# Kernel tuning notes

Hardware: AMD Instinct MI355X
Metric: run time of the kernel (lower is better)

Reference implementation:

```python
import jax, jax.numpy as jnp
import numpy as np

D_MODEL = 1024
H = 16
D_K = D_MODEL // H
D_FF = 4096
EPS = 1e-6
NEG = -1e9


def layernorm(x, alpha, bias):
    # custom LN: unbiased std (ddof=1), scalar alpha/bias, divide by (std+eps)
    mean = jnp.mean(x, axis=-1, keepdims=True)
    n = x.shape[-1]
    var = jnp.sum((x - mean) ** 2, axis=-1, keepdims=True) / (n - 1)
    std = jnp.sqrt(var)
    return alpha * (x - mean) / (std + EPS) + bias


def setup_inputs() -> dict:
    key = jax.random.key(0)
    ks = jax.random.split(key, 16)
    B, S = 2, 2048
    s = 1.0 / np.sqrt(D_MODEL)
    inp = {
        "x": jax.random.normal(ks[0], (B, S, D_MODEL), jnp.float32),
        "src_mask": jnp.ones((B, 1, S), jnp.int32),
        "wq": jax.random.normal(ks[1], (D_MODEL, D_MODEL), jnp.float32) * s,
        "bq": jnp.zeros((D_MODEL,), jnp.float32),
        "wk": jax.random.normal(ks[2], (D_MODEL, D_MODEL), jnp.float32) * s,
        "bk": jnp.zeros((D_MODEL,), jnp.float32),
        "wv": jax.random.normal(ks[3], (D_MODEL, D_MODEL), jnp.float32) * s,
        "bv": jnp.zeros((D_MODEL,), jnp.float32),
        "wo": jax.random.normal(ks[4], (D_MODEL, D_MODEL), jnp.float32) * s,
        "bo": jnp.zeros((D_MODEL,), jnp.float32),
        "w1": jax.random.normal(ks[5], (D_MODEL, D_FF), jnp.float32) * s,
        "b1": jnp.zeros((D_FF,), jnp.float32),
        "w2": jax.random.normal(ks[6], (D_FF, D_MODEL), jnp.float32) * (1.0 / np.sqrt(D_FF)),
        "b2": jnp.zeros((D_MODEL,), jnp.float32),
        "ln1_a": jnp.ones((1,), jnp.float32),
        "ln1_b": jnp.zeros((1,), jnp.float32),
        "ln2_a": jnp.ones((1,), jnp.float32),
        "ln2_b": jnp.zeros((1,), jnp.float32),
    }
    return inp


def reference(x, src_mask, wq, bq, wk, bk, wv, bv, wo, bo,
              w1, b1, w2, b2, ln1_a, ln1_b, ln2_a, ln2_b):
    B, S, _ = x.shape
    # --- residual 1: pre-norm self attention ---
    xn = layernorm(x, ln1_a, ln1_b)
    q = (xn @ wq + bq).reshape(B, S, H, D_K)
    k = (xn @ wk + bk).reshape(B, S, H, D_K)
    v = (xn @ wv + bv).reshape(B, S, H, D_K)
    # scores [B, H, S, S]
    scores = jnp.einsum("bqhd,bkhd->bhqk", q, k) / jnp.sqrt(jnp.float32(D_K))
    m = src_mask[:, None, :, :]  # [B,1,1,S]
    scores = jnp.where(m == 0, NEG, scores)
    attn = jax.nn.softmax(scores, axis=-1)
    ctx = jnp.einsum("bhqk,bkhd->bqhd", attn, v).reshape(B, S, D_MODEL)
    attn_out = ctx @ wo + bo
    x = x + attn_out
    # --- residual 2: pre-norm FFN ---
    xn = layernorm(x, ln2_a, ln2_b)
    ff = jax.nn.relu(xn @ w1 + b1) @ w2 + b2
    return x + ff
```

## Files before the change

kernel.cpp:

```cpp
#include <hip/hip_runtime.h>
#include <hip/hip_bf16.h>

typedef __attribute__((ext_vector_type(8))) short short8;
typedef __attribute__((ext_vector_type(4))) float f32x4;
typedef __attribute__((ext_vector_type(4))) unsigned int u32x4;
using u16 = unsigned short;
typedef unsigned int u32;

__device__ __forceinline__ u16 f2bf(float f) {
    u32 u = __builtin_bit_cast(u32, f);
    u32 r = u + 0x7FFFu + ((u >> 16) & 1u);
    return (u16)(r >> 16);
}

__device__ __forceinline__ float exp2fast(float x) {
    return __builtin_amdgcn_exp2f(x);
}

__device__ __forceinline__ u32 cvtpk(float lo, float hi) {
    u32 r;
    asm("v_cvt_pk_bf16_f32 %0, %1, %2" : "=v"(r) : "v"(lo), "v"(hi));
    return r;
}

__device__ __forceinline__ void async_load16(const void* g, void* l) {
    __builtin_amdgcn_global_load_lds(
        (const __attribute__((address_space(1))) void*)g,
        (__attribute__((address_space(3))) void*)l, 16, 0, 0);
}

__device__ __forceinline__ void wg_barrier() {
    asm volatile("" ::: "memory");
    __builtin_amdgcn_s_barrier();
    asm volatile("" ::: "memory");
}

__global__ __launch_bounds__(256) void convt_kernel(const float* __restrict__ w,
                                                    u16* __restrict__ wt, int K, int N) {
    __shared__ float tile[32][33];
    int bn = blockIdx.x * 32, bk = blockIdx.y * 32;
    int tx = threadIdx.x & 31, ty = threadIdx.x >> 5;
#pragma unroll
    for (int i = 0; i < 4; i++)
        tile[ty + i * 8][tx] = w[(size_t)(bk + ty + i * 8) * N + bn + tx];
    __syncthreads();
#pragma unroll
    for (int i = 0; i < 4; i++)
        wt[(size_t)(bn + ty + i * 8) * K + bk + tx] = f2bf(tile[tx][ty + i * 8]);
}

__global__ __launch_bounds__(256) void convt4_kernel(const float* __restrict__ wa,
                                                     const float* __restrict__ wb,
                                                     const float* __restrict__ wc,
                                                     const float* __restrict__ wd,
                                                     u16* __restrict__ da,
                                                     u16* __restrict__ db,
                                                     u16* __restrict__ dc,
                                                     u16* __restrict__ dd) {
    __shared__ float tile[32][33];
    int z = blockIdx.z;
    const float* w = (z == 0) ? wa : (z == 1) ? wb : (z == 2) ? wc : wd;
    u16* wt = (z == 0) ? da : (z == 1) ? db : (z == 2) ? dc : dd;
    int bn = blockIdx.x * 32, bk = blockIdx.y * 32;
    int tx = threadIdx.x & 31, ty = threadIdx.x >> 5;
#pragma unroll
    for (int i = 0; i < 4; i++)
        tile[ty + i * 8][tx] = w[(size_t)(bk + ty + i * 8) * 1024 + bn + tx];
    __syncthreads();
#pragma unroll
    for (int i = 0; i < 4; i++)
        wt[(size_t)(bn + ty + i * 8) * 1024 + bk + tx] = f2bf(tile[tx][ty + i * 8]);
}

__global__ __launch_bounds__(256) void vtrans_kernel(const u16* __restrict__ qkv,
                                                     u16* __restrict__ vT) {
    __shared__ u16 tile[32][33];
    int bs = blockIdx.x * 32;
    int bc = blockIdx.y * 32;
    int b  = blockIdx.z;
    int tx = threadIdx.x & 31, ty = threadIdx.x >> 5;
#pragma unroll
    for (int i = 0; i < 4; i++)
        tile[ty + i * 8][tx] = qkv[(size_t)(b * 2048 + bs + ty + i * 8) * 3072 + 2048 + bc + tx];
    __syncthreads();
#pragma unroll
    for (int i = 0; i < 4; i++)
        vT[(size_t)(b * 1024 + bc + ty + i * 8) * 2048 + bs + tx] = tile[tx][ty + i * 8];
}

__global__ __launch_bounds__(256) void ln_kernel(const float* __restrict__ x,
                                                 const float* __restrict__ ga,
                                                 const float* __restrict__ gb,
                                                 u16* __restrict__ out) {
    int row = blockIdx.x;
    const float4* xr = (const float4*)(x + (size_t)row * 1024);
    float4 v = xr[threadIdx.x];
    float s  = v.x + v.y + v.z + v.w;
    float s2 = v.x * v.x + v.y * v.y + v.z * v.z + v.w * v.w;
#pragma unroll
    for (int off = 32; off; off >>= 1) {
        s  += __shfl_down(s, off);
        s2 += __shfl_down(s2, off);
    }
    __shared__ float rs[4], rs2[4];
    int wid = threadIdx.x >> 6, lane = threadIdx.x & 63;
    if (lane == 0) { rs[wid] = s; rs2[wid] = s2; }
    __syncthreads();
    float S  = rs[0] + rs[1] + rs[2] + rs[3];
    float S2 = rs2[0] + rs2[1] + rs2[2] + rs2[3];
    float mean = S * (1.0f / 1024.0f);
    float var  = fmaxf((S2 - 1024.0f * mean * mean) * (1.0f / 1023.0f), 0.0f);
    float scale = ga[0] / (sqrtf(var) + 1e-6f);
    float shift = gb[0] - mean * scale;
    u16 h0 = f2bf(v.x * scale + shift);
    u16 h1 = f2bf(v.y * scale + shift);
    u16 h2 = f2bf(v.z * scale + shift);
    u16 h3 = f2bf(v.w * scale + shift);
    uint2 pv;
    pv.x = (u32)h0 | ((u32)h1 << 16);
    pv.y = (u32)h2 | ((u32)h3 << 16);
    *(uint2*)(out + (size_t)row * 1024 + threadIdx.x * 4) = pv;
}

__global__ __launch_bounds__(256) void bias3_kernel(const float* __restrict__ a,
                                                    const float* __restrict__ b,
                                                    const float* __restrict__ c,
                                                    float* __restrict__ d) {
    int i = blockIdx.x * 256 + threadIdx.x;
    float v = (i < 1024) ? a[i] : ((i < 2048) ? b[i - 1024] : c[i - 2048]);
    d[i] = v;
}

__global__ __launch_bounds__(256) void addbias_kernel(float* __restrict__ dst,
                                                      const float* __restrict__ p,
                                                      const float* __restrict__ bias,
                                                      const float* __restrict__ resid) {
    int i4 = blockIdx.x * 256 + threadIdx.x;
    float4 d  = ((const float4*)dst)[i4];
    float4 pp = ((const float4*)p)[i4];
    float4 rr = ((const float4*)resid)[i4];
    float4 bb = *(const float4*)(bias + ((i4 * 4) & 1023));
    d.x += pp.x + bb.x + rr.x;
    d.y += pp.y + bb.y + rr.y;
    d.z += pp.z + bb.z + rr.z;
    d.w += pp.w + bb.w + rr.w;
    ((float4*)dst)[i4] = d;
}

__global__ __launch_bounds__(256) void addbias2_ln_kernel(float* __restrict__ dst,
                                                          const float* __restrict__ p0,
                                                          const float* __restrict__ p1,
                                                          const float* __restrict__ bias,
                                                          const float* __restrict__ resid,
                                                          const float* __restrict__ ga,
                                                          const float* __restrict__ gb,
                                                          u16* __restrict__ xn) {
    int row = blockIdx.x;
    int i4 = row * 256 + threadIdx.x;
    float4 d  = ((const float4*)dst)[i4];
    float4 pa = ((const float4*)p0)[i4];
    float4 pb = ((const float4*)p1)[i4];
    float4 rr = ((const float4*)resid)[i4];
    float4 bb = *(const float4*)(bias + threadIdx.x * 4);
    d.x += pa.x + pb.x + bb.x + rr.x;
    d.y += pa.y + pb.y + bb.y + rr.y;
    d.z += pa.z + pb.z + bb.z + rr.z;
    d.w += pa.w + pb.w + bb.w + rr.w;
    ((float4*)dst)[i4] = d;

    float s  = d.x + d.y + d.z + d.w;
    float s2 = d.x * d.x + d.y * d.y + d.z * d.z + d.w * d.w;
#pragma unroll
    for (int off = 32; off; off >>= 1) {
        s  += __shfl_down(s, off);
        s2 += __shfl_down(s2, off);
    }
    __shared__ float rs[4], rs2[4];
    int wid = threadIdx.x >> 6, lane = threadIdx.x & 63;
    if (lane == 0) { rs[wid] = s; rs2[wid] = s2; }
    __syncthreads();
    float S  = rs[0] + rs[1] + rs[2] + rs[3];
    float S2 = rs2[0] + rs2[1] + rs2[2] + rs2[3];
    float mean = S * (1.0f / 1024.0f);
    float var  = fmaxf((S2 - 1024.0f * mean * mean) * (1.0f / 1023.0f), 0.0f);
    float scale = ga[0] / (sqrtf(var) + 1e-6f);
    float shift = gb[0] - mean * scale;
    uint2 pv;
    pv.x = (u32)f2bf(d.x * scale + shift) | ((u32)f2bf(d.y * scale + shift) << 16);
    pv.y = (u32)f2bf(d.z * scale + shift) | ((u32)f2bf(d.w * scale + shift) << 16);
    *(uint2*)(xn + (size_t)row * 1024 + threadIdx.x * 4) = pv;
}

template <int RELU>
__global__ __launch_bounds__(512) void gemm256_bt(const u16* __restrict__ A,
                                                  const u16* __restrict__ Bt,
                                                  const float* __restrict__ bias,
                                                  u16* __restrict__ C,
                                                  int M, int N, int K, int tilesN) {
    __shared__ u16 lds[2][2][16384];
    const int tid = threadIdx.x;
    const int lane = tid & 63, wid = tid >> 6;
    const int l15 = lane & 15, l4 = lane >> 4;
    const int wm = wid >> 2, wn = wid & 3;

    int nwg = gridDim.x;
    int bid = blockIdx.x;
    int swz = (bid & 7) * (nwg >> 3) + (bid >> 3);
    int ty = swz / tilesN, tx = swz % tilesN;

    const u16* Ag = A + (size_t)(ty * 256) * K;
    const u16* Bg = Bt + (size_t)(tx * 256) * K;

    auto stage_half = [&](int slot, int ab, int half, const u16* G, int k0) {
#pragma unroll
        for (int j = 0; j < 2; j++) {
            int off16 = half * 1024 + j * 512 + tid;
            int r = off16 >> 3;
            int gs = (off16 & 7) ^ (r & 7);
            const u16* src = G + (size_t)r * K + k0 + gs * 8;
            u16* dst = &lds[slot][ab][(size_t)(half * 1024 + j * 512 + (wid << 6)) * 8];
            async_load16(src, dst);
        }
    };

    f32x4 acc[8][4] = {};
    const int nT = K >> 6;

    stage_half(0, 0, 0, Ag, 0);
    stage_half(0, 0, 1, Ag, 0);
    stage_half(0, 1, 0, Bg, 0);
    stage_half(0, 1, 1, Bg, 0);
    __builtin_amdgcn_sched_barrier(0);

    for (int t = 0; t < nT; ++t) {
        const int cs = t & 1, ns = cs ^ 1;
        const int k1 = (t + 1) << 6;
        const bool pf = (t + 1 < nT);
#pragma unroll
        for (int ph = 0; ph < 4; ++ph) {
            if (ph == 0 && pf) { stage_half(ns, 0, 0, Ag, k1); stage_half(ns, 0, 1, Ag, k1); }
            if (ph == 1 && pf) { stage_half(ns, 1, 0, Bg, k1); stage_half(ns, 1, 1, Bg, k1); }
            __builtin_amdgcn_sched_barrier(0);
            if (ph == 0) {
                if (pf) asm volatile("s_waitcnt vmcnt(4)" ::: "memory");
                else    asm volatile("s_waitcnt vmcnt(0)" ::: "memory");
            }
            wg_barrier();

            const int rh = ph >> 1, ch = ph & 1;
            const u16* la = &lds[cs][0][0];
            const u16* lb = &lds[cs][1][0];
            short8 af[4][2], bf[2][2];
#pragma unroll
            for (int m2 = 0; m2 < 4; m2++) {
                int ra = wm * 128 + rh * 64 + m2 * 16 + l15;
#pragma unroll
                for (int ks = 0; ks < 2; ks++) {
                    int sl = (l4 + ks * 4) ^ (ra & 7);
                    af[m2][ks] = *(const short8*)&la[ra * 64 + sl * 8];
                }
            }
#pragma unroll
            for (int n2 = 0; n2 < 2; n2++) {
                int rb = wn * 64 + ch * 32 + n2 * 16 + l15;
#pragma unroll
                for (int ks = 0; ks < 2; ks++) {
                    int sl = (l4 + ks * 4) ^ (rb & 7);
                    bf[n2][ks] = *(const short8*)&lb[rb * 64 + sl * 8];
                }
            }
            __builtin_amdgcn_s_setprio(1);
#pragma unroll
            for (int m2 = 0; m2 < 4; m2++)
#pragma unroll
                for (int n2 = 0; n2 < 2; n2++)
#pragma unroll
                    for (int ks = 0; ks < 2; ks++)
                        acc[rh * 4 + m2][ch * 2 + n2] = __builtin_amdgcn_mfma_f32_16x16x32_bf16(
                            af[m2][ks], bf[n2][ks], acc[rh * 4 + m2][ch * 2 + n2], 0, 0, 0);
            __builtin_amdgcn_s_setprio(0);
            wg_barrier();
        }
    }

#pragma unroll
    for (int mi = 0; mi < 8; mi++) {
        int row0 = ty * 256 + wm * 128 + (mi >> 2) * 64 + (mi & 3) * 16 + l4 * 4;
#pragma unroll
        for (int ni = 0; ni < 4; ni++) {
            int col = tx * 256 + wn * 64 + (ni >> 1) * 32 + (ni & 1) * 16 + l15;
            float bc = bias[col];
#pragma unroll
            for (int jj = 0; jj < 4; jj++) {
                float v = acc[mi][ni][jj] + bc;
                if (RELU) v = fmaxf(v, 0.0f);
                C[(size_t)(row0 + jj) * N + col] = f2bf(v);
            }
        }
    }
}

template <int MODE, int RELU, int RESID>
__global__ __launch_bounds__(256) void gemm_bt(const u16* __restrict__ A,
                                               const u16* __restrict__ Bt,
                                               const float* __restrict__ bias,
                                               void* __restrict__ C0,
                                               void* __restrict__ C1,
                                               void* __restrict__ Cp1,
                                               const float* __restrict__ resid,
                                               int M, int N, int K, int kLen) {
    __shared__ u16 As[8192];
    __shared__ u16 Bs[8192];
    int tid = threadIdx.x, lane = tid & 63, wid = tid >> 6;
    int l15 = lane & 15, l4 = lane >> 4;
    int rowA0 = blockIdx.x * 128;
    int rowB0 = blockIdx.y * 128;
    int kOff = blockIdx.z * kLen;
    int len = K - kOff; if (len > kLen) len = kLen;
    void* Cout = (blockIdx.z == gridDim.z - 1) ? C1 : (blockIdx.z == 0 ? C0 : Cp1);
    int waveM = wid >> 1, waveN = wid & 1;

    int fl = tid * 8;
    int r0 = fl >> 5, c0 = fl & 31;
    const u16* gA0 = A + (size_t)(rowA0 + r0) * K + c0 + kOff;
    const u16* gA1 = A + (size_t)(rowA0 + 64 + r0) * K + c0 + kOff;
    const u16* gB0 = Bt + (size_t)(rowB0 + r0) * K + c0 + kOff;
    const u16* gB1 = Bt + (size_t)(rowB0 + 64 + r0) * K + c0 + kOff;

    f32x4 acc[4][4] = {};
    const int nIter = len >> 5;

    async_load16(gA0, As + wid * 512);
    async_load16(gA1, As + 2048 + wid * 512);
    async_load16(gB0, Bs + wid * 512);
    async_load16(gB1, Bs + 2048 + wid * 512);

    int cur = 0, kb = 32;
    for (int it = 0; it < nIter; ++it) {
        asm volatile("s_waitcnt vmcnt(0)" ::: "memory");
        __builtin_amdgcn_s_barrier();
        if (it + 1 < nIter) {
            u16* a = As + (cur ^ 1) * 4096;
            u16* bb = Bs + (cur ^ 1) * 4096;
            async_load16(gA0 + kb, a + wid * 512);
            async_load16(gA1 + kb, a + 2048 + wid * 512);
            async_load16(gB0 + kb, bb + wid * 512);
            async_load16(gB1 + kb, bb + 2048 + wid * 512);
        }
        __builtin_amdgcn_sched_barrier(0);

        const u16* a = As + cur * 4096;
        const u16* bb = Bs + cur * 4096;
        short8 af[4], bf[4];
#pragma unroll
        for (int m = 0; m < 4; m++)
            af[m] = *(const short8*)&a[(waveM * 64 + m * 16 + l15) * 32 + l4 * 8];
#pragma unroll
        for (int n = 0; n < 4; n++)
            bf[n] = *(const short8*)&bb[(waveN * 64 + n * 16 + l15) * 32 + l4 * 8];
#pragma unroll
        for (int m = 0; m < 4; m++)
#pragma unroll
            for (int n = 0; n < 4; n++)
                acc[m][n] = __builtin_amdgcn_mfma_f32_16x16x32_bf16(af[m], bf[n], acc[m][n], 0, 0, 0);

        __builtin_amdgcn_s_barrier();
        cur ^= 1;
        kb += 32;
    }

#pragma unroll
    for (int m = 0; m < 4; m++) {
        int row = rowA0 + waveM * 64 + m * 16 + l4 * 4;
#pragma unroll
        for (int n = 0; n < 4; n++) {
            int col = rowB0 + waveN * 64 + n * 16 + l15;
            float bc = (MODE == 2) ? 0.0f : bias[col];
#pragma unroll
            for (int j = 0; j < 4; j++) {
                float v = acc[m][n][j] + bc;
                if (RELU) v = fmaxf(v, 0.0f);
                if (RESID) v += resid[(size_t)(row + j) * N + col];
                if (MODE == 1)
                    ((u16*)Cout)[(size_t)(row + j) * N + col] = f2bf(v);
                else
                    ((float*)Cout)[(size_t)(row + j) * N + col] = v;
            }
        }
    }
}

__global__ __launch_bounds__(512) void attn_kernel(const u16* __restrict__ qkv,
                                                   const u16* __restrict__ vT,
                                                   const int* __restrict__ mask,
                                                   u16* __restrict__ ctx) {
    const int S = 2048;
    const float C = 0.180336880f;
    int qt = blockIdx.x;
    int bh = blockIdx.y;
    int b = bh >> 4, h = bh & 15;
    int tid = threadIdx.x;
    int wid = tid >> 6, lane = tid & 63;
    int l15 = lane & 15, l4 = lane >> 4;
    int g = wid >> 2, qw = wid & 3;

    __shared__ u16 Ks[2][64][72];
    __shared__ u16 Vs[2][64][72];
    __shared__ u32 PT[8][16][38];
    __shared__ float mbuf[2][4][16], lbuf[2][4][16];
    __shared__ int mflag;

    if (tid == 0) mflag = 1;
    __syncthreads();
    {
        const int* mrow = mask + b * S;
        int ok = 1;
#pragma unroll
        for (int i = 0; i < 4; i++) ok &= (mrow[tid * 4 + i] != 0);
        if (!ok) mflag = 0;
    }

    int qrow0 = qt * 64 + qw * 16;
    const u16* qb = qkv + (size_t)(b * S + qrow0) * 3072 + h * 64;
    short8 qf0 = *(const short8*)(qb + (size_t)l15 * 3072 + l4 * 8);
    short8 qf1 = *(const short8*)(qb + (size_t)l15 * 3072 + 32 + l4 * 8);

    f32x4 o[4] = {};
    float m_i = -1e30f, lp = 0.0f;
    __syncthreads();
    const int allones = mflag;
    const int* mrow = mask + b * S;

    int tl = tid & 255;
    int srow = tl >> 3, c8 = (tl & 7) * 8;
    const int kt0 = g * 16;
    short8 kreg[2], vreg[2];
#pragma unroll
    for (int p = 0; p < 2; p++) {
        int r = p * 32 + srow;
        kreg[p] = *(const short8*)(qkv + (size_t)(b * S + kt0 * 64 + r) * 3072 + 1024 + h * 64 + c8);
        vreg[p] = *(const short8*)(vT + (size_t)(bh * 64 + r) * 2048 + kt0 * 64 + c8);
    }

    for (int it = 0; it < 16; ++it) {
        const int kt = kt0 + it;
        wg_barrier();
#pragma unroll
        for (int p = 0; p < 2; p++) {
            int r = p * 32 + srow;
            *(short8*)&Ks[g][r][c8] = kreg[p];
            *(short8*)&Vs[g][r][c8] = vreg[p];
        }
        if (it + 1 < 16) {
#pragma unroll
            for (int p = 0; p < 2; p++) {
                int r = p * 32 + srow;
                kreg[p] = *(const short8*)(qkv + (size_t)(b * S + (kt + 1) * 64 + r) * 3072 + 1024 + h * 64 + c8);
                vreg[p] = *(const short8*)(vT + (size_t)(bh * 64 + r) * 2048 + (kt + 1) * 64 + c8);
            }
        }
        asm volatile("s_waitcnt lgkmcnt(0)" ::: "memory");
        wg_barrier();

        float sc[4][4];
#pragma unroll
        for (int kc = 0; kc < 4; kc++) {
            short8 kf0 = *(const short8*)&Ks[g][kc * 16 + l15][l4 * 8];
            short8 kf1 = *(const short8*)&Ks[g][kc * 16 + l15][32 + l4 * 8];
            f32x4 a = {};
            a = __builtin_amdgcn_mfma_f32_16x16x32_bf16(kf0, qf0, a, 0, 0, 0);
            a = __builtin_amdgcn_mfma_f32_16x16x32_bf16(kf1, qf1, a, 0, 0, 0);
            if (allones) {
#pragma unroll
                for (int j = 0; j < 4; j++) sc[kc][j] = a[j];
            } else {
#pragma unroll
                for (int j = 0; j < 4; j++) {
                    int mk = mrow[kt * 64 + kc * 16 + l4 * 4 + j];
                    sc[kc][j] = mk ? a[j] : -1e9f;
                }
            }
        }

        float lm = sc[0][0];
#pragma unroll
        for (int kc = 0; kc < 4; kc++)
#pragma unroll
            for (int j = 0; j < 4; j++) lm = fmaxf(lm, sc[kc][j]);
        if (!__all(lm <= m_i + 64.0f)) {
            float t = lm;
            t = fmaxf(t, __shfl_xor(t, 16));
            t = fmaxf(t, __shfl_xor(t, 32));
            float newm = fmaxf(m_i, t);
            float r = exp2fast((m_i - newm) * C);
            lp *= r;
            float rr0 = __shfl(r, l4 * 4 + 0);
            float rr1 = __shfl(r, l4 * 4 + 1);
            float rr2 = __shfl(r, l4 * 4 + 2);
            float rr3 = __shfl(r, l4 * 4 + 3);
#pragma unroll
            for (int dc = 0; dc < 4; dc++) {
                o[dc][0] *= rr0; o[dc][1] *= rr1; o[dc][2] *= rr2; o[dc][3] *= rr3;
            }
            m_i = newm;
        }

        float nb = -m_i * C;
#pragma unroll
        for (int kc = 0; kc < 4; kc++) {
            float p0 = exp2fast(fmaf(sc[kc][0], C, nb));
            float p1 = exp2fast(fmaf(sc[kc][1], C, nb));
            float p2 = exp2fast(fmaf(sc[kc][2], C, nb));
            float p3 = exp2fast(fmaf(sc[kc][3], C, nb));
            lp += (p0 + p1) + (p2 + p3);
            uint2 w;
            w.x = cvtpk(p0, p1);
            w.y = cvtpk(p2, p3);
            *(uint2*)&PT[wid][l15][kc * 8 + l4 * 2] = w;
        }

        uint2 r01 = *(const uint2*)&PT[wid][l15][l4 * 4];
        uint2 r23 = *(const uint2*)&PT[wid][l15][l4 * 4 + 2];
        uint2 r45 = *(const uint2*)&PT[wid][l15][16 + l4 * 4];
        uint2 r67 = *(const uint2*)&PT[wid][l15][16 + l4 * 4 + 2];
        u32x4 w0 = {r01.x, r01.y, r23.x, r23.y};
        u32x4 w1 = {r45.x, r45.y, r67.x, r67.y};
        short8 pa0 = __builtin_bit_cast(short8, w0);
        short8 pa1 = __builtin_bit_cast(short8, w1);

#pragma unroll
        for (int dc = 0; dc < 4; dc++) {
            short8 vf0 = *(const short8*)&Vs[g][dc * 16 + l15][l4 * 8];
            short8 vf1 = *(const short8*)&Vs[g][dc * 16 + l15][32 + l4 * 8];
            o[dc] = __builtin_amdgcn_mfma_f32_16x16x32_bf16(pa0, vf0, o[dc], 0, 0, 0);
            o[dc] = __builtin_amdgcn_mfma_f32_16x16x32_bf16(pa1, vf1, o[dc], 0, 0, 0);
        }
    }

    float lt = lp;
    lt += __shfl_xor(lt, 16);
    lt += __shfl_xor(lt, 32);
    if (l4 == 0) { mbuf[g][qw][l15] = m_i; lbuf[g][qw][l15] = lt; }
    __syncthreads();
    float mo = mbuf[g ^ 1][qw][l15], lo = lbuf[g ^ 1][qw][l15];
    float M  = fmaxf(m_i, mo);
    float rs = exp2fast((m_i - M) * C);
    float ro = exp2fast((mo - M) * C);
    float inv = 1.0f / (rs * lt + ro * lo);
    float rs_j[4], iv_j[4];
#pragma unroll
    for (int j = 0; j < 4; j++) {
        rs_j[j] = __shfl(rs,  l4 * 4 + j);
        iv_j[j] = __shfl(inv, l4 * 4 + j);
    }

    float* obuf = (float*)&Ks[0][0][0];
#pragma unroll
    for (int c = 0; c < 2; c++) {
        int dce = (g ^ 1) * 2 + c;
#pragma unroll
        for (int j = 0; j < 4; j++)
            obuf[(((g * 4 + qw) * 16) + l4 * 4 + j) * 32 + c * 16 + l15] = o[dce][j] * rs_j[j];
    }
    __syncthreads();
#pragma unroll
    for (int c = 0; c < 2; c++) {
        int dco = g * 2 + c;
#pragma unroll
        for (int j = 0; j < 4; j++) {
            float peer = obuf[((((g ^ 1) * 4 + qw) * 16) + l4 * 4 + j) * 32 + c * 16 + l15];
            float val = (o[dco][j] * rs_j[j] + peer) * iv_j[j];
            int row = qrow0 + l4 * 4 + j;
            ctx[(size_t)(b * S + row) * 1024 + h * 64 + dco * 16 + l15] = f2bf(val);
        }
    }
}

extern "C" void kernel_launch(void* const* d_in, const int* in_sizes, int n_in,
                              void* d_out, int out_size, void* d_ws, size_t ws_size,
                              hipStream_t stream) {
    const float* x    = (const float*)d_in[0];
    const int*   mask = (const int*)d_in[1];
    const float* wq   = (const float*)d_in[2];
    const float* bq   = (const float*)d_in[3];
    const float* wk   = (const float*)d_in[4];
    const float* bk   = (const float*)d_in[5];
    const float* wv   = (const float*)d_in[6];
    const float* bv   = (const float*)d_in[7];
    const float* wo   = (const float*)d_in[8];
    const float* bo   = (const float*)d_in[9];
    const float* w1   = (const float*)d_in[10];
    const float* b1   = (const float*)d_in[11];
    const float* w2   = (const float*)d_in[12];
    const float* b2   = (const float*)d_in[13];
    const float* ln1a = (const float*)d_in[14];
    const float* ln1b = (const float*)d_in[15];
    const float* ln2a = (const float*)d_in[16];
    const float* ln2b = (const float*)d_in[17];
    float* out = (float*)d_out;

    char* ws = (char*)d_ws;
    u16*   wqkvt = (u16*)(ws + 0);
    u16*   wot   = (u16*)(ws + 6291456);
    u16*   w1t   = (u16*)(ws + 8388608);
    u16*   w2t   = (u16*)(ws + 16777216);
    float* bqkv  = (float*)(ws + 25165824);
    char*  regA  = ws + 26214400;
    u16*   xn1   = (u16*)(regA + 0);
    u16*   vT    = (u16*)(regA + 0);
    u16*   qkv   = (u16*)(regA + 8388608);
    u16*   ctx   = (u16*)(regA + 33554432);
    float* p0wo  = (float*)(regA + 0);
    float* p1wo  = (float*)(regA + 16777216);
    float* x1    = (float*)(ws + 68157440);
    u16*   xn2   = (u16*)(regA + 0);
    u16*   ff1   = (u16*)(regA + 8388608);
    float* p0f2  = (float*)(ws + 0);

    dim3 blk(256);

    convt4_kernel<<<dim3(32, 32, 4), blk, 0, stream>>>(
        wq, wk, wv, wo, wqkvt, wqkvt + 1024 * 1024, wqkvt + 2048 * 1024, wot);
    convt_kernel<<<dim3(128, 32), blk, 0, stream>>>(w1, w1t, 1024, 4096);
    convt_kernel<<<dim3(32, 128), blk, 0, stream>>>(w2, w2t, 4096, 1024);
    bias3_kernel<<<dim3(12), blk, 0, stream>>>(bq, bk, bv, bqkv);

    ln_kernel<<<dim3(4096), blk, 0, stream>>>(x, ln1a, ln1b, xn1);
    gemm256_bt<0><<<dim3(192), dim3(512), 0, stream>>>(xn1, wqkvt, bqkv, qkv, 4096, 3072, 1024, 12);
    vtrans_kernel<<<dim3(64, 32, 2), blk, 0, stream>>>(qkv, vT);
    attn_kernel<<<dim3(32, 32), dim3(512), 0, stream>>>(qkv, vT, mask, ctx);
    gemm_bt<2, 0, 0><<<dim3(32, 8, 3), blk, 0, stream>>>(ctx, wot, nullptr, p0wo, x1, p1wo,
                                                         nullptr, 4096, 1024, 1024, 352);
    addbias2_ln_kernel<<<dim3(4096), blk, 0, stream>>>(x1, p0wo, p1wo, bo, x, ln2a, ln2b, xn2);

    gemm256_bt<1><<<dim3(256), dim3(512), 0, stream>>>(xn2, w1t, b1, ff1, 4096, 4096, 1024, 16);
    gemm_bt<2, 0, 0><<<dim3(32, 8, 2), blk, 0, stream>>>(ff1, w2t, nullptr, p0f2, out, nullptr,
                                                         nullptr, 4096, 1024, 4096, 2048);
    addbias_kernel<<<dim3(4096), blk, 0, stream>>>(out, p0f2, b2, x1);
}
```

Before: 271.3 us.

## Run FFN down-projection on 256x256 split-K GEMM with bf16 partials

The FFN second GEMM (K=4096) now runs on the larger 256x256 tile kernel, with split-K across 4 slices instead of the 128-tile kernel with 2-way split. Three slices write bf16 partial sums and the last writes fp32 into the output. A reduction kernel sums the bf16 partials with bias and residual. The aim is more reuse per tile and less partial-sum traffic. The bf16 partials lose some precision.

```diff
diff --git a/kernel.cpp b/kernel.cpp
--- a/kernel.cpp
+++ b/kernel.cpp
@@ -11,6 +11,13 @@
     u32 u = __builtin_bit_cast(u32, f);
     u32 r = u + 0x7FFFu + ((u >> 16) & 1u);
     return (u16)(r >> 16);
+}
+
+__device__ __forceinline__ float bf2f(u32 w) {
+    return __builtin_bit_cast(float, w << 16);
+}
+__device__ __forceinline__ float bf2f_hi(u32 w) {
+    return __builtin_bit_cast(float, w & 0xFFFF0000u);
 }
 
 __device__ __forceinline__ float exp2fast(float x) {
@@ -131,19 +138,23 @@
     d[i] = v;
 }
 
-__global__ __launch_bounds__(256) void addbias_kernel(float* __restrict__ dst,
-                                                      const float* __restrict__ p,
-                                                      const float* __restrict__ bias,
-                                                      const float* __restrict__ resid) {
+__global__ __launch_bounds__(256) void addbias3b_kernel(float* __restrict__ dst,
+                                                        const u16* __restrict__ p0,
+                                                        const u16* __restrict__ p1,
+                                                        const u16* __restrict__ p2,
+                                                        const float* __restrict__ bias,
+                                                        const float* __restrict__ resid) {
     int i4 = blockIdx.x * 256 + threadIdx.x;
     float4 d  = ((const float4*)dst)[i4];
-    float4 pp = ((const float4*)p)[i4];
+    uint2 ua = ((const uint2*)p0)[i4];
+    uint2 ub = ((const uint2*)p1)[i4];
+    uint2 uc = ((const uint2*)p2)[i4];
     float4 rr = ((const float4*)resid)[i4];
     float4 bb = *(const float4*)(bias + ((i4 * 4) & 1023));
-    d.x += pp.x + bb.x + rr.x;
-    d.y += pp.y + bb.y + rr.y;
-    d.z += pp.z + bb.z + rr.z;
-    d.w += pp.w + bb.w + rr.w;
+    d.x += bf2f(ua.x) + bf2f(ub.x) + bf2f(uc.x) + bb.x + rr.x;
+    d.y += bf2f_hi(ua.x) + bf2f_hi(ub.x) + bf2f_hi(uc.x) + bb.y + rr.y;
+    d.z += bf2f(ua.y) + bf2f(ub.y) + bf2f(uc.y) + bb.z + rr.z;
+    d.w += bf2f_hi(ua.y) + bf2f_hi(ub.y) + bf2f_hi(uc.y) + bb.w + rr.w;
     ((float4*)dst)[i4] = d;
 }
 
@@ -191,12 +202,16 @@
     *(uint2*)(xn + (size_t)row * 1024 + threadIdx.x * 4) = pv;
 }
 
-template <int RELU>
+template <int MODE, int RELU>
 __global__ __launch_bounds__(512) void gemm256_bt(const u16* __restrict__ A,
                                                   const u16* __restrict__ Bt,
                                                   const float* __restrict__ bias,
                                                   u16* __restrict__ C,
-                                                  int M, int N, int K, int tilesN) {
+                                                  u16* __restrict__ P0,
+                                                  u16* __restrict__ P1,
+                                                  u16* __restrict__ P2,
+                                                  float* __restrict__ Cf,
+                                                  int M, int N, int K, int tilesN, int kLen) {
     __shared__ u16 lds[2][2][16384];
     const int tid = threadIdx.x;
     const int lane = tid & 63, wid = tid >> 6;
@@ -207,6 +222,7 @@
     int bid = blockIdx.x;
     int swz = (bid & 7) * (nwg >> 3) + (bid >> 3);
     int ty = swz / tilesN, tx = swz % tilesN;
+    const int kOff = blockIdx.y * kLen;
 
     const u16* Ag = A + (size_t)(ty * 256) * K;
     const u16* Bg = Bt + (size_t)(tx * 256) * K;
@@ -224,17 +240,17 @@
     };
 
     f32x4 acc[8][4] = {};
-    const int nT = K >> 6;
-
-    stage_half(0, 0, 0, Ag, 0);
-    stage_half(0, 0, 1, Ag, 0);
-    stage_half(0, 1, 0, Bg, 0);
-    stage_half(0, 1, 1, Bg, 0);
+    const int nT = kLen >> 6;
+
+    stage_half(0, 0, 0, Ag, kOff);
+    stage_half(0, 0, 1, Ag, kOff);
+    stage_half(0, 1, 0, Bg, kOff);
+    stage_half(0, 1, 1, Bg, kOff);
     __builtin_amdgcn_sched_barrier(0);
 
     for (int t = 0; t < nT; ++t) {
         const int cs = t & 1, ns = cs ^ 1;
-        const int k1 = (t + 1) << 6;
+        const int k1 = kOff + ((t + 1) << 6);
         const bool pf = (t + 1 < nT);
 #pragma unroll
         for (int ph = 0; ph < 4; ++ph) {
@@ -283,18 +299,38 @@
         }
     }
 
-#pragma unroll
-    for (int mi = 0; mi < 8; mi++) {
-        int row0 = ty * 256 + wm * 128 + (mi >> 2) * 64 + (mi & 3) * 16 + l4 * 4;
-#pragma unroll
-        for (int ni = 0; ni < 4; ni++) {
-            int col = tx * 256 + wn * 64 + (ni >> 1) * 32 + (ni & 1) * 16 + l15;
-            float bc = bias[col];
-#pragma unroll
-            for (int jj = 0; jj < 4; jj++) {
-                float v = acc[mi][ni][jj] + bc;
-                if (RELU) v = fmaxf(v, 0.0f);
-                C[(size_t)(row0 + jj) * N + col] = f2bf(v);
+    if (MODE == 0) {
+#pragma unroll
+        for (int mi = 0; mi < 8; mi++) {
+            int row0 = ty * 256 + wm * 128 + (mi >> 2) * 64 + (mi & 3) * 16 + l4 * 4;
+#pragma unroll
+            for (int ni = 0; ni < 4; ni++) {
+                int col = tx * 256 + wn * 64 + (ni >> 1) * 32 + (ni & 1) * 16 + l15;
+                float bc = bias[col];
+#pragma unroll
+                for (int jj = 0; jj < 4; jj++) {
+                    float v = acc[mi][ni][jj] + bc;
+                    if (RELU) v = fmaxf(v, 0.0f);
+                    C[(size_t)(row0 + jj) * N + col] = f2bf(v);
+                }
+            }
+        }
+    } else {
+        int z = blockIdx.y;
+        bool last = (z == gridDim.y - 1);
+        u16* P = (z == 0) ? P0 : (z == 1) ? P1 : P2;
+#pragma unroll
+        for (int mi = 0; mi < 8; mi++) {
+            int row0 = ty * 256 + wm * 128 + (mi >> 2) * 64 + (mi & 3) * 16 + l4 * 4;
+#pragma unroll
+            for (int ni = 0; ni < 4; ni++) {
+                int col = tx * 256 + wn * 64 + (ni >> 1) * 32 + (ni & 1) * 16 + l15;
+#pragma unroll
+                for (int jj = 0; jj < 4; jj++) {
+                    float v = acc[mi][ni][jj];
+                    if (last) Cf[(size_t)(row0 + jj) * N + col] = v;
+                    else      P[(size_t)(row0 + jj) * N + col] = f2bf(v);
+                }
             }
         }
     }
@@ -615,7 +651,9 @@
     float* x1    = (float*)(ws + 68157440);
     u16*   xn2   = (u16*)(regA + 0);
     u16*   ff1   = (u16*)(regA + 8388608);
-    float* p0f2  = (float*)(ws + 0);
+    u16*   pb0   = (u16*)(ws + 0);
+    u16*   pb1   = (u16*)(ws + 8388608);
+    u16*   pb2   = (u16*)(regA + 0);
 
     dim3 blk(256);
 
@@ -626,15 +664,17 @@
     bias3_kernel<<<dim3(12), blk, 0, stream>>>(bq, bk, bv, bqkv);
 
     ln_kernel<<<dim3(4096), blk, 0, stream>>>(x, ln1a, ln1b, xn1);
-    gemm256_bt<0><<<dim3(192), dim3(512), 0, stream>>>(xn1, wqkvt, bqkv, qkv, 4096, 3072, 1024, 12);
+    gemm256_bt<0, 0><<<dim3(192, 1), dim3(512), 0, stream>>>(
+        xn1, wqkvt, bqkv, qkv, nullptr, nullptr, nullptr, nullptr, 4096, 3072, 1024, 12, 1024);
     vtrans_kernel<<<dim3(64, 32, 2), blk, 0, stream>>>(qkv, vT);
     attn_kernel<<<dim3(32, 32), dim3(512), 0, stream>>>(qkv, vT, mask, ctx);
     gemm_bt<2, 0, 0><<<dim3(32, 8, 3), blk, 0, stream>>>(ctx, wot, nullptr, p0wo, x1, p1wo,
                                                          nullptr, 4096, 1024, 1024, 352);
     addbias2_ln_kernel<<<dim3(4096), blk, 0, stream>>>(x1, p0wo, p1wo, bo, x, ln2a, ln2b, xn2);
 
-    gemm256_bt<1><<<dim3(256), dim3(512), 0, stream>>>(xn2, w1t, b1, ff1, 4096, 4096, 1024, 16);
-    gemm_bt<2, 0, 0><<<dim3(32, 8, 2), blk, 0, stream>>>(ff1, w2t, nullptr, p0f2, out, nullptr,
-                                                         nullptr, 4096, 1024, 4096, 2048);
-    addbias_kernel<<<dim3(4096), blk, 0, stream>>>(out, p0f2, b2, x1);
-}
+    gemm256_bt<0, 1><<<dim3(256, 1), dim3(512), 0, stream>>>(
+        xn2, w1t, b1, ff1, nullptr, nullptr, nullptr, nullptr, 4096, 4096, 1024, 16, 1024);
+    gemm256_bt<2, 0><<<dim3(64, 4), dim3(512), 0, stream>>>(
+        ff1, w2t, nullptr, nullptr, pb0, pb1, pb2, out, 4096, 1024, 4096, 4, 1024);
+    addbias3b_kernel<<<dim3(4096), blk, 0, stream>>>(out, pb0, pb1, pb2, b2, x1);
+}
```

Measured after the change: 263.6 us. 1.03x faster.
